# Kernel tuning notes

Hardware: AMD Instinct MI355X
Metric: run time of the kernel (lower is better)

The kernel has to match this reference:

```python
import jax, jax.numpy as jnp
import numpy as np

N_EXPERTS = 64
TOP_K = 4
D_MODEL = 512
D_FF = 2048
B, T = 2, 1024


def setup_inputs() -> dict:
    key = jax.random.key(0)
    k1, k2, k3, k4 = jax.random.split(key, 4)
    x = jax.random.normal(k1, (B, T, D_MODEL), dtype=jnp.float32)
    hex_weights = jax.random.uniform(k2, (B, T, N_EXPERTS), dtype=jnp.float32)
    W_in = jax.random.normal(k3, (N_EXPERTS, D_FF, D_MODEL), dtype=jnp.float32) * (D_MODEL ** -0.5)
    W_out = jax.random.normal(k4, (N_EXPERTS, D_MODEL, D_FF), dtype=jnp.float32) * (D_FF ** -0.5)
    bias_in = jnp.zeros((N_EXPERTS, D_FF), dtype=jnp.float32)
    bias_out = jnp.zeros((N_EXPERTS, D_MODEL), dtype=jnp.float32)
    return {"x": x, "hex_weights": hex_weights, "W_in": W_in, "bias_in": bias_in,
            "W_out": W_out, "bias_out": bias_out}


def reference(x, hex_weights, W_in, bias_in, W_out, bias_out):
    # x: (B,T,D); hex_weights: (B,T,64)
    Bv, Tv, D = x.shape
    N = Bv * Tv
    xf = x.reshape(N, D)
    hw = hex_weights.reshape(N, N_EXPERTS)
    top_w, top_idx = jax.lax.top_k(hw, TOP_K)                 # (N,K)
    top_w = top_w / (jnp.sum(top_w, axis=-1, keepdims=True) + 1e-8)
    # Sparse combine matrix: row n has top_w at selected experts, 0 elsewhere.
    combine = jnp.zeros((N, N_EXPERTS), dtype=x.dtype).at[
        jnp.arange(N)[:, None], top_idx].add(top_w)            # (N,64)
    # Scan over the 64 experts; equivalent math to per-token weight gather,
    # since combine is zero for unselected experts.
    def body(acc, ew):
        Wi, bi, Wo, bo, c = ew                                 # Wi:(d_ff,D), c:(N,)
        h = jax.nn.silu(xf @ Wi.T + bi)                        # (N,d_ff)
        o = h @ Wo.T + bo                                      # (N,D)
        return acc + c[:, None] * o, None
    out, _ = jax.lax.scan(body, jnp.zeros_like(xf),
                          (W_in, bias_in, W_out, bias_out, combine.T))
    return out.reshape(Bv, Tv, D)
```

## Files before the change

kernel.cpp:

```cpp
#include <hip/hip_runtime.h>
#include <hip/hip_bf16.h>
#include <stdint.h>

#define NTOK 2048
#define NE 64
#define TOPK 4
#define DM 512
#define DF 2048
#define TOTSLOT (NTOK*TOPK)

#define BM 192
#define BN 128
#define BK 64
#define GEMM_GRID 1024

typedef __bf16 bf16;
typedef __bf16 bf16x8 __attribute__((ext_vector_type(8)));
typedef __bf16 bf16x4 __attribute__((ext_vector_type(4)));
typedef float  f32x4  __attribute__((ext_vector_type(4)));
typedef short  short8 __attribute__((ext_vector_type(8)));


__global__ void k_route(const float* __restrict__ hw, float* __restrict__ top_w,
                        int* __restrict__ top_idx) {
  int t = blockIdx.x * blockDim.x + threadIdx.x;
  if (t >= NTOK) return;
  const float* r = hw + (size_t)t * NE;
  float rv[NE];
  #pragma unroll
  for (int e = 0; e < NE; ++e) rv[e] = r[e];
  float v[TOPK]; int id[TOPK];
  #pragma unroll
  for (int k = 0; k < TOPK; ++k) {
    float best = -1e30f; int bi = 0;
    #pragma unroll
    for (int e = 0; e < NE; ++e) {
      bool used = false;
      #pragma unroll
      for (int j = 0; j < k; ++j) used |= (id[j] == e);
      if (!used && rv[e] > best) { best = rv[e]; bi = e; }
    }
    v[k] = best; id[k] = bi;
  }
  float den = v[0] + v[1] + v[2] + v[3] + 1e-8f;
  #pragma unroll
  for (int k = 0; k < TOPK; ++k) {
    top_w[t*TOPK + k] = v[k] / den;
    top_idx[t*TOPK + k] = id[k];
  }
}

__global__ __launch_bounds__(256) void k_build(
    const int* __restrict__ top_idx, int* __restrict__ tok,
    int* __restrict__ slot_of, int* __restrict__ offsets_g,
    int* __restrict__ tasklist, int* __restrict__ ntask_g) {
  __shared__ int cnt_s[NE], off_s[NE + 1], fill_s[NE], tpre_s[NE + 1];
  const int tid = threadIdx.x;
  if (tid < NE) { cnt_s[tid] = 0; fill_s[tid] = 0; }
  __syncthreads();
  int ids[TOTSLOT / 256];
  #pragma unroll
  for (int c = 0; c < TOTSLOT / 256; ++c) {
    ids[c] = top_idx[c * 256 + tid];
    atomicAdd(&cnt_s[ids[c]], 1);
  }
  __syncthreads();
  if (tid < 64) {
    int c = cnt_s[tid];
    int inc = c;
    #pragma unroll
    for (int d = 1; d < 64; d <<= 1) {
      int n = __shfl_up(inc, d, 64);
      if (tid >= d) inc += n;
    }
    off_s[tid] = inc - c;
    if (tid == 63) off_s[64] = inc;

    int tc = (c + BM - 1) / BM;
    int tinc = tc;
    #pragma unroll
    for (int d = 1; d < 64; d <<= 1) {
      int n = __shfl_up(tinc, d, 64);
      if (tid >= d) tinc += n;
    }
    tpre_s[tid] = tinc - tc;
    if (tid == 63) tpre_s[64] = tinc;
  }
  __syncthreads();
  #pragma unroll
  for (int c = 0; c < TOTSLOT / 256; ++c) {
    int idx = c * 256 + tid;
    int e = ids[c];
    int pos = off_s[e] + atomicAdd(&fill_s[e], 1);
    tok[pos] = idx >> 2;
    slot_of[idx] = pos;
  }
  if (tid < 64) {
    int tc = (cnt_s[tid] + BM - 1) / BM;
    int base = tpre_s[tid];
    for (int m = 0; m < tc; ++m) tasklist[base + m] = (tid << 8) | m;
    if (tid == 0) *ntask_g = tpre_s[64];
  }
  if (tid <= NE) offsets_g[tid] = off_s[tid];
}

__global__ void k_xcast(const float* __restrict__ x, bf16* __restrict__ xb) {
  int i = blockIdx.x * blockDim.x + threadIdx.x;
  int base = i * 4;
  if (base >= NTOK * DM) return;
  float4 f = *(const float4*)(x + base);
  bf16x4 o;
  o[0] = (bf16)f.x; o[1] = (bf16)f.y; o[2] = (bf16)f.z; o[3] = (bf16)f.w;
  *(bf16x4*)(xb + base) = o;
}


template<int PASS, int KSPLIT>
__global__ __launch_bounds__(512) void k_gemm(
    const float* __restrict__ W, const float* __restrict__ bias,
    const bf16* __restrict__ Asrc, const int* __restrict__ tok,
    const int* __restrict__ offsets,
    const int* __restrict__ tasklist, const int* __restrict__ ntask_g,
    bf16* __restrict__ Hout, float* __restrict__ Oout)
{
  constexpr int KFULL = (PASS == 1) ? DM : DF;
  constexpr int KLOC  = KFULL / KSPLIT;
  constexpr int KT    = KLOC / BK;
  constexpr int NDIM  = (PASS == 1) ? DF : DM;
  constexpr int NT    = NDIM / BN;

  const int tid = threadIdx.x;
  const int wave = tid >> 6, lane = tid & 63;
  const int wm = wave >> 1, wn = wave & 1;
  const int lrow = lane >> 4, lcol = lane & 15;

  __shared__ bf16 As[BM * BK];
  __shared__ bf16 Bs[BN * BK];

  const int ntask = *ntask_g;
  const int NG = ntask * KSPLIT;
  const int gPerXcd = (NG + 7) / 8;
  const int tot = 8 * gPerXcd * NT;

  #pragma unroll 1
  for (int tt = blockIdx.x; tt < tot; tt += GEMM_GRID) {
    const int xcd  = tt & 7;
    const int v    = tt >> 3;
    const int gloc = v / NT;
    const int ntile= v % NT;
    const int g    = xcd * gPerXcd + gloc;
    if (g >= NG) continue;
    const int taskIdx = g / KSPLIT;
    const int ks      = g % KSPLIT;
    const int em = tasklist[taskIdx];
    const int e  = em >> 8;
    const int mt = em & 255;
    const int kbase = ks * KLOC;

    const int off = offsets[e];
    const int cnt = offsets[e+1] - off;
    const int rowcount = cnt - mt * BM;

    const bf16* abase[3]; bool aok[3];
    #pragma unroll
    for (int c = 0; c < 3; ++c) {
      int r = (c * 512 + tid) >> 3;
      aok[c] = (r < rowcount);
      int srcrow;
      if (PASS == 1) srcrow = aok[c] ? tok[off + mt*BM + r] : 0;
      else           srcrow = min(off + mt*BM + (aok[c] ? r : 0), TOTSLOT - 1);
      abase[c] = Asrc + (size_t)srcrow * KFULL + kbase + (tid & 7) * 8;
    }
    const int brow = tid >> 2;
    const float* bbase = W + (size_t)e * NDIM * KFULL
                           + (size_t)(ntile*BN + brow) * KFULL + kbase + (tid & 3) * 16;

    f32x4 acc[3][4];
    #pragma unroll
    for (int i = 0; i < 3; ++i)
      #pragma unroll
      for (int j = 0; j < 4; ++j) acc[i][j] = (f32x4)(0.0f);

    #pragma unroll 1
    for (int kt = 0; kt < KT; ++kt) {
      const int k0 = kt * BK;
      short8 areg[3];
      #pragma unroll
      for (int c = 0; c < 3; ++c) {
        if (PASS == 2 || aok[c]) areg[c] = *(const short8*)(abase[c] + k0);
        else                     areg[c] = (short8){0,0,0,0,0,0,0,0};
      }
      float4 breg[4];
      #pragma unroll
      for (int q = 0; q < 4; ++q) breg[q] = *(const float4*)(bbase + k0 + q*4);

      __syncthreads();
      #pragma unroll
      for (int c = 0; c < 3; ++c) {
        int r = (c * 512 + tid) >> 3;
        int u = tid & 7;
        *(short8*)(&As[r*BK + ((u ^ (r & 7)) * 8)]) = areg[c];
      }
      {
        const float* fv = (const float*)breg;
        bf16x8 p0, p1;
        #pragma unroll
        for (int q = 0; q < 8; ++q) { p0[q] = (bf16)fv[q]; p1[q] = (bf16)fv[q+8]; }
        int u0 = (tid & 3) * 2;
        *(bf16x8*)(&Bs[brow*BK + (((u0  ) ^ (brow & 7)) * 8)]) = p0;
        *(bf16x8*)(&Bs[brow*BK + (((u0+1) ^ (brow & 7)) * 8)]) = p1;
      }
      __syncthreads();

      #pragma unroll
      for (int ksub = 0; ksub < 2; ++ksub) {
        const int uu = ksub*4 + lrow;
        bf16x8 af[3], bfr[4];
        #pragma unroll
        for (int i = 0; i < 3; ++i) {
          int m = wm*48 + i*16 + lcol;
          af[i] = *(const bf16x8*)(&As[m*BK + ((uu ^ (m & 7)) * 8)]);
        }
        #pragma unroll
        for (int j = 0; j < 4; ++j) {
          int n = wn*64 + j*16 + lcol;
          bfr[j] = *(const bf16x8*)(&Bs[n*BK + ((uu ^ (n & 7)) * 8)]);
        }
        #pragma unroll
        for (int i = 0; i < 3; ++i)
          #pragma unroll
          for (int j = 0; j < 4; ++j)
            acc[i][j] = __builtin_amdgcn_mfma_f32_16x16x32_bf16(af[i], bfr[j], acc[i][j], 0, 0, 0);
      }
    }

    const int slotbase = off + mt * BM;
    #pragma unroll
    for (int i = 0; i < 3; ++i) {
      const int rbase = wm*48 + i*16 + lrow*4;
      #pragma unroll
      for (int j = 0; j < 4; ++j) {
        const int gcol = ntile*BN + wn*64 + j*16 + lcol;
        const float bv = (PASS == 2 && ks != 0) ? 0.0f : bias[(size_t)e * NDIM + gcol];
        #pragma unroll
        for (int q = 0; q < 4; ++q) {
          const int r = rbase + q;
          if (r < rowcount) {
            float h = acc[i][j][q] + bv;
            if (PASS == 1) {
              float s = h / (1.0f + __expf(-h));
              Hout[(size_t)(slotbase + r) * DF + gcol] = (bf16)s;
            } else {
              Oout[(size_t)ks * TOTSLOT * DM + (size_t)(slotbase + r) * DM + gcol] = h;
            }
          }
        }
      }
    }
    __syncthreads();
  }
}


__global__ void k_combine(const float* __restrict__ O, const float* __restrict__ top_w,
                          const int* __restrict__ slot_of, float* __restrict__ out) {
  int i = blockIdx.x * blockDim.x + threadIdx.x;
  if (i >= NTOK * DM / 4) return;
  int t  = i / (DM / 4);
  int d4 = (i % (DM / 4)) * 4;
  float4 s = {0.f, 0.f, 0.f, 0.f};
  #pragma unroll
  for (int k = 0; k < TOPK; ++k) {
    float w = top_w[t*TOPK + k];
    int  sl = slot_of[t*TOPK + k];
    float sx = 0.f, sy = 0.f, sz = 0.f, sw = 0.f;
    #pragma unroll
    for (int p = 0; p < 4; ++p) {
      float4 o = *(const float4*)(O + (size_t)p * TOTSLOT * DM + (size_t)sl * DM + d4);
      sx += o.x; sy += o.y; sz += o.z; sw += o.w;
    }
    s.x += w * sx; s.y += w * sy; s.z += w * sz; s.w += w * sw;
  }
  *(float4*)(out + (size_t)t * DM + d4) = s;
}


extern "C" void kernel_launch(void* const* d_in, const int* in_sizes, int n_in,
                              void* d_out, int out_size, void* d_ws, size_t ws_size,
                              hipStream_t stream) {
  const float* x        = (const float*)d_in[0];
  const float* hw       = (const float*)d_in[1];
  const float* W_in     = (const float*)d_in[2];
  const float* bias_in  = (const float*)d_in[3];
  const float* W_out    = (const float*)d_in[4];
  const float* bias_out = (const float*)d_in[5];
  float* out = (float*)d_out;

  char* ws = (char*)d_ws;
  int*   offsets  = (int*)  (ws + 0);
  int*   ntask    = (int*)  (ws + 512);
  int*   tasklist = (int*)  (ws + 768);
  int*   top_idx  = (int*)  (ws + 2048);
  float* top_w    = (float*)(ws + 2048 + 32768);
  int*   slot_of  = (int*)  (ws + 2048 + 2*32768);
  int*   tok      = (int*)  (ws + 2048 + 3*32768);
  bf16*  xb       = (bf16*) (ws + 2048 + 4*32768);
  size_t o_xb_end = 2048 + 4*32768 + (size_t)NTOK*DM*2;
  bf16*  H        = (bf16*) (ws + o_xb_end);
  size_t o_H_end  = o_xb_end + (size_t)TOTSLOT*DF*2;
  float* O        = (float*)(ws + o_H_end);

  k_route<<<NTOK/256, 256, 0, stream>>>(hw, top_w, top_idx);
  k_build<<<1, 256, 0, stream>>>(top_idx, tok, slot_of, offsets, tasklist, ntask);
  k_xcast<<<(NTOK*DM/4)/256, 256, 0, stream>>>(x, xb);

  k_gemm<1,1><<<GEMM_GRID, 512, 0, stream>>>(W_in, bias_in, xb, tok, offsets,
                                             tasklist, ntask, H, nullptr);
  k_gemm<2,4><<<GEMM_GRID, 512, 0, stream>>>(W_out, bias_out, H, nullptr, offsets,
                                             tasklist, ntask, nullptr, O);

  k_combine<<<(NTOK*DM/4)/256, 256, 0, stream>>>(O, top_w, slot_of, out);
}
```

Measured before the change: 203.1 us.

## Replace split-K in down-projection GEMM with narrow N tiles

The second expert GEMM no longer splits the 2048-long K dimension four ways. It now parallelises over narrower 32-column output tiles that run the full K loop, which removes the four partial-sum buffers and makes the combine kernel read a single output slab. The B-tile load and LDS layout are generalised to a templated tile width. The narrow tiles reload the A operand (the H rows) 16 times per expert tile instead of 4, and give each wave fewer MFMAs per LDS load.

```diff
diff --git a/kernel.cpp b/kernel.cpp
--- a/kernel.cpp
+++ b/kernel.cpp
@@ -10,7 +10,6 @@
 #define TOTSLOT (NTOK*TOPK)
 
 #define BM 192
-#define BN 128
 #define BK 64
 #define GEMM_GRID 1024
 
@@ -115,7 +114,7 @@
 }
 
 
-template<int PASS, int KSPLIT>
+template<int PASS, int BNT>
 __global__ __launch_bounds__(512) void k_gemm(
     const float* __restrict__ W, const float* __restrict__ bias,
     const bf16* __restrict__ Asrc, const int* __restrict__ tok,
@@ -124,10 +123,12 @@
     bf16* __restrict__ Hout, float* __restrict__ Oout)
 {
   constexpr int KFULL = (PASS == 1) ? DM : DF;
-  constexpr int KLOC  = KFULL / KSPLIT;
-  constexpr int KT    = KLOC / BK;
+  constexpr int KT    = KFULL / BK;
   constexpr int NDIM  = (PASS == 1) ? DF : DM;
-  constexpr int NT    = NDIM / BN;
+  constexpr int NT    = NDIM / BNT;
+  constexpr int TPR   = 512 / BNT;
+  constexpr int NQ    = 16 / TPR;
+  constexpr int NJ    = BNT / 32;
 
   const int tid = threadIdx.x;
   const int wave = tid >> 6, lane = tid & 63;
@@ -135,11 +136,10 @@
   const int lrow = lane >> 4, lcol = lane & 15;
 
   __shared__ bf16 As[BM * BK];
-  __shared__ bf16 Bs[BN * BK];
+  __shared__ bf16 Bs[BNT * BK];
 
   const int ntask = *ntask_g;
-  const int NG = ntask * KSPLIT;
-  const int gPerXcd = (NG + 7) / 8;
+  const int gPerXcd = (ntask + 7) / 8;
   const int tot = 8 * gPerXcd * NT;
 
   #pragma unroll 1
@@ -149,13 +149,10 @@
     const int gloc = v / NT;
     const int ntile= v % NT;
     const int g    = xcd * gPerXcd + gloc;
-    if (g >= NG) continue;
-    const int taskIdx = g / KSPLIT;
-    const int ks      = g % KSPLIT;
-    const int em = tasklist[taskIdx];
+    if (g >= ntask) continue;
+    const int em = tasklist[g];
     const int e  = em >> 8;
     const int mt = em & 255;
-    const int kbase = ks * KLOC;
 
     const int off = offsets[e];
     const int cnt = offsets[e+1] - off;
@@ -169,17 +166,18 @@
       int srcrow;
       if (PASS == 1) srcrow = aok[c] ? tok[off + mt*BM + r] : 0;
       else           srcrow = min(off + mt*BM + (aok[c] ? r : 0), TOTSLOT - 1);
-      abase[c] = Asrc + (size_t)srcrow * KFULL + kbase + (tid & 7) * 8;
-    }
-    const int brow = tid >> 2;
+      abase[c] = Asrc + (size_t)srcrow * KFULL + (tid & 7) * 8;
+    }
+    const int brow = tid / TPR;
+    const int bseg = tid % TPR;
     const float* bbase = W + (size_t)e * NDIM * KFULL
-                           + (size_t)(ntile*BN + brow) * KFULL + kbase + (tid & 3) * 16;
-
-    f32x4 acc[3][4];
+                           + (size_t)(ntile*BNT + brow) * KFULL + bseg * (NQ*4);
+
+    f32x4 acc[3][NJ];
     #pragma unroll
     for (int i = 0; i < 3; ++i)
       #pragma unroll
-      for (int j = 0; j < 4; ++j) acc[i][j] = (f32x4)(0.0f);
+      for (int j = 0; j < NJ; ++j) acc[i][j] = (f32x4)(0.0f);
 
     #pragma unroll 1
     for (int kt = 0; kt < KT; ++kt) {
@@ -190,9 +188,9 @@
         if (PASS == 2 || aok[c]) areg[c] = *(const short8*)(abase[c] + k0);
         else                     areg[c] = (short8){0,0,0,0,0,0,0,0};
       }
-      float4 breg[4];
-      #pragma unroll
-      for (int q = 0; q < 4; ++q) breg[q] = *(const float4*)(bbase + k0 + q*4);
+      float4 breg[NQ];
+      #pragma unroll
+      for (int q = 0; q < NQ; ++q) breg[q] = *(const float4*)(bbase + k0 + q*4);
 
       __syncthreads();
       #pragma unroll
@@ -201,35 +199,35 @@
         int u = tid & 7;
         *(short8*)(&As[r*BK + ((u ^ (r & 7)) * 8)]) = areg[c];
       }
-      {
-        const float* fv = (const float*)breg;
-        bf16x8 p0, p1;
-        #pragma unroll
-        for (int q = 0; q < 8; ++q) { p0[q] = (bf16)fv[q]; p1[q] = (bf16)fv[q+8]; }
-        int u0 = (tid & 3) * 2;
-        *(bf16x8*)(&Bs[brow*BK + (((u0  ) ^ (brow & 7)) * 8)]) = p0;
-        *(bf16x8*)(&Bs[brow*BK + (((u0+1) ^ (brow & 7)) * 8)]) = p1;
+      #pragma unroll
+      for (int q = 0; q < NQ; ++q) {
+        bf16x4 p;
+        p[0] = (bf16)breg[q].x; p[1] = (bf16)breg[q].y;
+        p[2] = (bf16)breg[q].z; p[3] = (bf16)breg[q].w;
+        int s = bseg * NQ + q;
+        int unit = s >> 1, half = s & 1;
+        *(bf16x4*)((char*)&Bs[0] + brow*128 + ((unit ^ (brow & 7)) * 16) + half*8) = p;
       }
       __syncthreads();
 
       #pragma unroll
       for (int ksub = 0; ksub < 2; ++ksub) {
         const int uu = ksub*4 + lrow;
-        bf16x8 af[3], bfr[4];
+        bf16x8 af[3], bfr[NJ];
         #pragma unroll
         for (int i = 0; i < 3; ++i) {
           int m = wm*48 + i*16 + lcol;
           af[i] = *(const bf16x8*)(&As[m*BK + ((uu ^ (m & 7)) * 8)]);
         }
         #pragma unroll
-        for (int j = 0; j < 4; ++j) {
-          int n = wn*64 + j*16 + lcol;
+        for (int j = 0; j < NJ; ++j) {
+          int n = wn*(BNT/2) + j*16 + lcol;
           bfr[j] = *(const bf16x8*)(&Bs[n*BK + ((uu ^ (n & 7)) * 8)]);
         }
         #pragma unroll
         for (int i = 0; i < 3; ++i)
           #pragma unroll
-          for (int j = 0; j < 4; ++j)
+          for (int j = 0; j < NJ; ++j)
             acc[i][j] = __builtin_amdgcn_mfma_f32_16x16x32_bf16(af[i], bfr[j], acc[i][j], 0, 0, 0);
       }
     }
@@ -239,9 +237,9 @@
     for (int i = 0; i < 3; ++i) {
       const int rbase = wm*48 + i*16 + lrow*4;
       #pragma unroll
-      for (int j = 0; j < 4; ++j) {
-        const int gcol = ntile*BN + wn*64 + j*16 + lcol;
-        const float bv = (PASS == 2 && ks != 0) ? 0.0f : bias[(size_t)e * NDIM + gcol];
+      for (int j = 0; j < NJ; ++j) {
+        const int gcol = ntile*BNT + wn*(BNT/2) + j*16 + lcol;
+        const float bv = bias[(size_t)e * NDIM + gcol];
         #pragma unroll
         for (int q = 0; q < 4; ++q) {
           const int r = rbase + q;
@@ -251,7 +249,7 @@
               float s = h / (1.0f + __expf(-h));
               Hout[(size_t)(slotbase + r) * DF + gcol] = (bf16)s;
             } else {
-              Oout[(size_t)ks * TOTSLOT * DM + (size_t)(slotbase + r) * DM + gcol] = h;
+              Oout[(size_t)(slotbase + r) * DM + gcol] = h;
             }
           }
         }
@@ -273,13 +271,8 @@
   for (int k = 0; k < TOPK; ++k) {
     float w = top_w[t*TOPK + k];
     int  sl = slot_of[t*TOPK + k];
-    float sx = 0.f, sy = 0.f, sz = 0.f, sw = 0.f;
-    #pragma unroll
-    for (int p = 0; p < 4; ++p) {
-      float4 o = *(const float4*)(O + (size_t)p * TOTSLOT * DM + (size_t)sl * DM + d4);
-      sx += o.x; sy += o.y; sz += o.z; sw += o.w;
-    }
-    s.x += w * sx; s.y += w * sy; s.z += w * sz; s.w += w * sw;
+    float4 o = *(const float4*)(O + (size_t)sl * DM + d4);
+    s.x += w * o.x; s.y += w * o.y; s.z += w * o.z; s.w += w * o.w;
   }
   *(float4*)(out + (size_t)t * DM + d4) = s;
 }
@@ -314,10 +307,10 @@
   k_build<<<1, 256, 0, stream>>>(top_idx, tok, slot_of, offsets, tasklist, ntask);
   k_xcast<<<(NTOK*DM/4)/256, 256, 0, stream>>>(x, xb);
 
-  k_gemm<1,1><<<GEMM_GRID, 512, 0, stream>>>(W_in, bias_in, xb, tok, offsets,
-                                             tasklist, ntask, H, nullptr);
-  k_gemm<2,4><<<GEMM_GRID, 512, 0, stream>>>(W_out, bias_out, H, nullptr, offsets,
-                                             tasklist, ntask, nullptr, O);
+  k_gemm<1,128><<<GEMM_GRID, 512, 0, stream>>>(W_in, bias_in, xb, tok, offsets,
+                                               tasklist, ntask, H, nullptr);
+  k_gemm<2,32><<<GEMM_GRID, 512, 0, stream>>>(W_out, bias_out, H, nullptr, offsets,
+                                              tasklist, ntask, nullptr, O);
 
   k_combine<<<(NTOK*DM/4)/256, 256, 0, stream>>>(O, top_w, slot_of, out);
 }
```

New measurement: 209.2 us. +3.0%, slower.
